# Kernel optimization log

Hardware: AMD Instinct MI355X
Metric: run time of the kernel (lower is better)

The kernel has to match this reference:

```python
import jax, jax.numpy as jnp
import numpy as np

B, T, C, H = 1024, 256, 384, 64  # batch, block_size, n_embd, head_size


def _rope_tables():
    # standard rotary tables: theta_i = 10000^(-2i/H), angles = pos * theta
    inv_freq = 1.0 / (10000.0 ** (jnp.arange(0, H, 2, dtype=jnp.float32) / H))  # [H/2]
    pos = jnp.arange(T, dtype=jnp.float32)
    ang = pos[:, None] * inv_freq[None, :]          # [T, H/2]
    ang = jnp.concatenate([ang, ang], axis=-1)       # [T, H]
    return jnp.cos(ang), jnp.sin(ang)


def setup_inputs() -> dict:
    key = jax.random.key(0)
    kx, kq, kk, kv = jax.random.split(key, 4)
    cos, sin = _rope_tables()
    s = 1.0 / np.sqrt(C)
    return {
        "x": jax.random.normal(kx, (B, T, C), dtype=jnp.float32),
        "cos": cos,
        "sin": sin,
        "Wq": jax.random.normal(kq, (C, H), dtype=jnp.float32) * s,
        "Wk": jax.random.normal(kk, (C, H), dtype=jnp.float32) * s,
        "Wv": jax.random.normal(kv, (C, H), dtype=jnp.float32) * s,
    }


def _rotary(x, cos, sin):
    # x: [B, T, H]; cos/sin: [T, H]
    half = x.shape[-1] // 2
    x1, x2 = x[..., :half], x[..., half:]
    rotated = jnp.concatenate([-x2, x1], axis=-1)
    return x * cos + rotated * sin


def reference(x, cos, sin, Wq, Wk, Wv):
    Tn = x.shape[1]
    q = x @ Wq                                  # [B,T,H]
    k = x @ Wk
    v = x @ Wv
    q = _rotary(q, cos[:Tn], sin[:Tn])
    k = _rotary(k, cos[:Tn], sin[:Tn])
    scale = k.shape[-1] ** -0.5
    wei = jnp.einsum('btd,bsd->bts', q, k) * scale  # [B,T,T] — materialized as in original
    causal = jnp.tril(jnp.ones((Tn, Tn), dtype=bool))
    wei = jnp.where(causal, wei, -jnp.inf)
    wei = jax.nn.softmax(wei, axis=-1)
    # dropout omitted (eval mode / deterministic reference)
    out = jnp.einsum('bts,bsd->btd', wei, v)    # [B,T,H]
    return out
```

## Files before the change

### kernel.cpp

```cpp
#include <hip/hip_runtime.h>
#include <hip/hip_bf16.h>


typedef __attribute__((ext_vector_type(8))) short bf16x8;
typedef __attribute__((ext_vector_type(4))) float f32x4;

#define B_ 1024
#define T_ 256
#define C_ 384
#define H_ 64

static __device__ __forceinline__ unsigned short f2bf(float f) {
  unsigned int u = __float_as_uint(f);
  return (unsigned short)((u + 0x7fffu + ((u >> 16) & 1u)) >> 16);
}

static __device__ __forceinline__ float bf2f(unsigned short h) {
  return __uint_as_float(((unsigned int)h) << 16);
}

static __device__ __forceinline__ bf16x8 cvt8(float4 a, float4 b) {
  union { __hip_bfloat162 h[4]; bf16x8 v; } u;
  u.h[0] = __float22bfloat162_rn(make_float2(a.x, a.y));
  u.h[1] = __float22bfloat162_rn(make_float2(a.z, a.w));
  u.h[2] = __float22bfloat162_rn(make_float2(b.x, b.y));
  u.h[3] = __float22bfloat162_rn(make_float2(b.z, b.w));
  return u.v;
}

__global__ void pack_w_frag(const float* __restrict__ Wq, const float* __restrict__ Wk,
                            const float* __restrict__ Wv, unsigned short* __restrict__ wtp) {
  int id = blockIdx.x * 256 + threadIdx.x;
  if (id >= 144 * 512) return;
  int i = id & 7, lane = (id >> 3) & 63, f = id >> 9;
  int nt = f % 12, ks = f / 12;
  int n = nt * 16 + (lane & 15);
  int k = ks * 32 + (lane >> 4) * 8 + i;
  const float* W = (n < 64) ? Wq : ((n < 128) ? Wk : Wv);
  wtp[id] = f2bf(W[k * 64 + (n & 63)]);
}

__launch_bounds__(256, 6)
__global__ void qkv_kernel(const float* __restrict__ x, const float* __restrict__ cosp,
                           const float* __restrict__ sinp,
                           const unsigned short* __restrict__ wtp,
                           unsigned short* __restrict__ qp,
                           unsigned short* __restrict__ kp,
                           unsigned short* __restrict__ vp) {
  __shared__ __align__(16) unsigned short xs[32 * 384];

  unsigned short* Qst = xs;
  unsigned short* Kst = xs + 2304;
  unsigned short* Vst = xs + 4608;

  const int tid = threadIdx.x;
  const int w = tid >> 6;
  const int lane = tid & 63;
  const int l15 = lane & 15;
  const int lq = lane >> 4;
  const int bk = blockIdx.x;
  const int b = bk >> 3, g32 = bk & 7;
  const int row0 = g32 * 32;

  const float* xb = x + (size_t)b * T_ * C_ + (size_t)row0 * C_;

  {
    float4 c0[2], c1[2];
    {
      const float* p = xb + (size_t)tid * 8;
      c0[0] = *(const float4*)p; c0[1] = *(const float4*)(p + 4);
    }
    #pragma unroll
    for (int s = 0; s < 6; ++s) {
      if (s + 1 < 6) {
        const float* p = xb + (size_t)((s + 1) * 256 + tid) * 8;
        c1[0] = *(const float4*)p; c1[1] = *(const float4*)(p + 4);
      }
      int c = s * 256 + tid;
      int row = c / 48;
      int cb = (c - row * 48) * 16;
      *(bf16x8*)((char*)xs + row * 768 + (cb ^ ((row & 7) << 4))) = cvt8(c0[0], c0[1]);
      c0[0] = c1[0]; c0[1] = c1[1];
    }
  }
  __syncthreads();

  const int ng = w;

  f32x4 acc[2][3];
  #pragma unroll
  for (int i = 0; i < 2; ++i)
    #pragma unroll
    for (int m = 0; m < 3; ++m) {
      f32x4 z = {0.f, 0.f, 0.f, 0.f};
      acc[i][m] = z;
    }

  const int arow0 = l15;
  const int arow1 = 16 + l15;
  const char* xrow0 = (const char*)xs + arow0 * 768;
  const char* xrow1 = (const char*)xs + arow1 * 768;
  const int asw0 = (arow0 & 7) << 4;
  const int asw1 = (arow1 & 7) << 4;

  #pragma unroll
  for (int ks = 0; ks < 12; ++ks) {
    bf16x8 bv[3];
    #pragma unroll
    for (int m = 0; m < 3; ++m)
      bv[m] = *(const bf16x8*)(wtp + ((size_t)(ks * 12 + ng * 3 + m) * 64 + lane) * 8);
    bf16x8 a0 = *(const bf16x8*)(xrow0 + ((ks * 64 + lq * 16) ^ asw0));
    bf16x8 a1 = *(const bf16x8*)(xrow1 + ((ks * 64 + lq * 16) ^ asw1));
    #pragma unroll
    for (int m = 0; m < 3; ++m) {
      acc[0][m] = __builtin_amdgcn_mfma_f32_16x16x32_bf16(a0, bv[m], acc[0][m], 0, 0, 0);
      acc[1][m] = __builtin_amdgcn_mfma_f32_16x16x32_bf16(a1, bv[m], acc[1][m], 0, 0, 0);
    }
  }
  __syncthreads();

  #pragma unroll
  for (int i = 0; i < 2; ++i) {
    #pragma unroll
    for (int m = 0; m < 3; ++m) {
      const int nt = ng * 3 + m;
      #pragma unroll
      for (int j = 0; j < 4; ++j) {
        const int r32 = i * 16 + lq * 4 + j;
        unsigned short v = f2bf(acc[i][m][j]);
        if (nt < 4)      Qst[r32 * 72 + nt * 16 + l15] = v;
        else if (nt < 8) Kst[r32 * 72 + (nt - 4) * 16 + l15] = v;
        else             Vst[((nt - 8) * 16 + l15) * 40 + r32] = v;
      }
    }
  }
  __syncthreads();

  #pragma unroll
  for (int pass = 0; pass < 3; ++pass) {
    const int id = pass * 4 + w;
    if (id < 8) {
      const unsigned short* S = (id < 4) ? Qst : Kst;
      unsigned short* dst = (id < 4) ? qp : kp;
      const int lid = id & 3;
      const int tl = lid >> 1;
      const int ks2 = lid & 1;
      const int r32 = tl * 16 + l15;
      const int c0 = ks2 * 32 + lq * 8;
      const unsigned short* rowp = S + r32 * 72;
      bf16x8 mv = *(const bf16x8*)(rowp + c0);
      bf16x8 pv = *(const bf16x8*)(rowp + (c0 ^ 32));
      const int tglob = row0 + r32;
      const float* cp = cosp + tglob * H_ + c0;
      const float* sp = sinp + tglob * H_ + c0;
      float4 ca = *(const float4*)cp, cb = *(const float4*)(cp + 4);
      float4 sa = *(const float4*)sp, sb = *(const float4*)(sp + 4);
      const float sgn = ks2 ? 1.0f : -1.0f;
      bf16x8 ov;
      ov[0] = (short)f2bf(bf2f((unsigned short)mv[0]) * ca.x + sgn * bf2f((unsigned short)pv[0]) * sa.x);
      ov[1] = (short)f2bf(bf2f((unsigned short)mv[1]) * ca.y + sgn * bf2f((unsigned short)pv[1]) * sa.y);
      ov[2] = (short)f2bf(bf2f((unsigned short)mv[2]) * ca.z + sgn * bf2f((unsigned short)pv[2]) * sa.z);
      ov[3] = (short)f2bf(bf2f((unsigned short)mv[3]) * ca.w + sgn * bf2f((unsigned short)pv[3]) * sa.w);
      ov[4] = (short)f2bf(bf2f((unsigned short)mv[4]) * cb.x + sgn * bf2f((unsigned short)pv[4]) * sb.x);
      ov[5] = (short)f2bf(bf2f((unsigned short)mv[5]) * cb.y + sgn * bf2f((unsigned short)pv[5]) * sb.y);
      ov[6] = (short)f2bf(bf2f((unsigned short)mv[6]) * cb.z + sgn * bf2f((unsigned short)pv[6]) * sb.z);
      ov[7] = (short)f2bf(bf2f((unsigned short)mv[7]) * cb.w + sgn * bf2f((unsigned short)pv[7]) * sb.w);
      const int tile_glob = g32 * 2 + tl;
      *(bf16x8*)(dst + ((((size_t)b * 16 + tile_glob) * 2 + ks2) * 64 + lane) * 8) = ov;
    } else if (id < 12) {
      const int ntv = id - 8;
      bf16x8 fr = *(const bf16x8*)(Vst + (ntv * 16 + l15) * 40 + lq * 8);
      *(bf16x8*)(vp + ((((size_t)b * 4 + ntv) * 8 + g32) * 64 + lane) * 8) = fr;
    }
  }
}

__launch_bounds__(256, 4)
__global__ void attn_kernel(const unsigned short* __restrict__ qp,
                            const unsigned short* __restrict__ kp,
                            const unsigned short* __restrict__ vp,
                            float* __restrict__ out) {
  __shared__ unsigned short Plds[4 * 16 * 264];

  const int tid = threadIdx.x;
  const int w = tid >> 6;
  const int lane = tid & 63;
  const int l15 = lane & 15;
  const int lq = lane >> 4;
  const int bk = blockIdx.x;
  const int b = bk >> 1, half = bk & 1;
  const int rt2[2] = {half * 8 + w, half * 8 + 7 - w};

  unsigned short* Pw = Plds + w * 16 * 264;
  float* ob = out + (size_t)b * T_ * H_;

  #pragma unroll
  for (int i = 0; i < 2; ++i) {
    const int ti = rt2[i];
    const int t0 = ti * 16;

    bf16x8 aq[2];
    #pragma unroll
    for (int ks2 = 0; ks2 < 2; ++ks2)
      aq[ks2] = *(const bf16x8*)(qp + ((((size_t)b * 16 + ti) * 2 + ks2) * 64 + lane) * 8);

    f32x4 sacc[16];
    #pragma unroll
    for (int si = 0; si < 16; ++si) {
      f32x4 z = {0.f, 0.f, 0.f, 0.f};
      sacc[si] = z;
    }

    #pragma unroll
    for (int si = 0; si < 16; ++si) {
      if (si <= ti) {
        #pragma unroll
        for (int ks2 = 0; ks2 < 2; ++ks2) {
          bf16x8 bkf = *(const bf16x8*)(kp + ((((size_t)b * 16 + si) * 2 + ks2) * 64 + lane) * 8);
          sacc[si] = __builtin_amdgcn_mfma_f32_16x16x32_bf16(aq[ks2], bkf, sacc[si], 0, 0, 0);
        }
      }
    }

    int trow = t0 + lq * 4;
    #pragma unroll
    for (int si = 0; si < 16; ++si) {
      #pragma unroll
      for (int j = 0; j < 4; ++j) {
        float s = sacc[si][j] * 0.125f;
        if (si * 16 + l15 > trow + j) s = -1e30f;
        sacc[si][j] = s;
      }
    }

    float rl[4];
    #pragma unroll
    for (int j = 0; j < 4; ++j) {
      float mj = -1e30f;
      #pragma unroll
      for (int si = 0; si < 16; ++si) mj = fmaxf(mj, sacc[si][j]);
      #pragma unroll
      for (int d = 1; d < 16; d <<= 1) mj = fmaxf(mj, __shfl_xor(mj, d));
      float lj = 0.0f;
      #pragma unroll
      for (int si = 0; si < 16; ++si) {
        float p = __expf(sacc[si][j] - mj);
        lj += p;
        Pw[(lq * 4 + j) * 264 + si * 16 + l15] = f2bf(p);
      }
      #pragma unroll
      for (int d = 1; d < 16; d <<= 1) lj += __shfl_xor(lj, d);
      rl[j] = 1.0f / lj;
    }

    f32x4 oacc[4];
    #pragma unroll
    for (int nt = 0; nt < 4; ++nt) {
      f32x4 z = {0.f, 0.f, 0.f, 0.f};
      oacc[nt] = z;
    }
    int nk = (t0 + 16 + 31) >> 5;
    for (int ks = 0; ks < nk; ++ks) {
      bf16x8 ap = *(const bf16x8*)&Pw[l15 * 264 + ks * 32 + lq * 8];
      #pragma unroll
      for (int nt = 0; nt < 4; ++nt) {
        bf16x8 bv = *(const bf16x8*)(vp + ((((size_t)b * 4 + nt) * 8 + ks) * 64 + lane) * 8);
        oacc[nt] = __builtin_amdgcn_mfma_f32_16x16x32_bf16(ap, bv, oacc[nt], 0, 0, 0);
      }
    }

    #pragma unroll
    for (int nt = 0; nt < 4; ++nt)
      #pragma unroll
      for (int j = 0; j < 4; ++j)
        ob[(t0 + lq * 4 + j) * H_ + nt * 16 + l15] = oacc[nt][j] * rl[j];
  }
}

extern "C" void kernel_launch(void* const* d_in, const int* in_sizes, int n_in,
                              void* d_out, int out_size, void* d_ws, size_t ws_size,
                              hipStream_t stream) {
  const float* x    = (const float*)d_in[0];
  const float* cosp = (const float*)d_in[1];
  const float* sinp = (const float*)d_in[2];
  const float* Wq   = (const float*)d_in[3];
  const float* Wk   = (const float*)d_in[4];
  const float* Wv   = (const float*)d_in[5];
  float* out = (float*)d_out;

  const size_t wtp_bytes = 144 * 512 * 2;
  const size_t frag_elems = (size_t)B_ * 16 * 2 * 64 * 8;

  unsigned short* wtp = (unsigned short*)d_ws;
  unsigned short* qp = (unsigned short*)((char*)d_ws + wtp_bytes);
  unsigned short* kp = qp + frag_elems;
  unsigned short* vp = kp + frag_elems;
  (void)ws_size;

  pack_w_frag<<<288, 256, 0, stream>>>(Wq, Wk, Wv, wtp);
  qkv_kernel<<<B_ * 8, 256, 0, stream>>>(x, cosp, sinp, wtp, qp, kp, vp);
  attn_kernel<<<B_ * 2, 256, 0, stream>>>(qp, kp, vp, out);
}
```

Before: 222.4 us.

## Stage fp32 x tile via direct global-to-LDS loads, convert to bf16 on read

Replaces the register-staged fp32-to-bf16 conversion of the x tile with async global_load_lds copies that write raw fp32 into LDS, using a swizzled source address so LDS reads stay conflict-free. The bf16 conversion moves into the MFMA loop, where each A fragment is built from two float4 LDS reads. This doubles LDS usage to 48KB per block, so launch bounds drop from 6 to 3 blocks per SM, trading occupancy for fewer VGPR round trips during the load. It also adds conversion work to the inner loop.

```diff
diff --git a/kernel.cpp b/kernel.cpp
--- a/kernel.cpp
+++ b/kernel.cpp
@@ -17,6 +17,11 @@
 
 static __device__ __forceinline__ float bf2f(unsigned short h) {
   return __uint_as_float(((unsigned int)h) << 16);
+}
+
+static __device__ __forceinline__ void glds16(const void* g, void* l) {
+  __builtin_amdgcn_global_load_lds((const __attribute__((address_space(1))) void*)g,
+                                   (__attribute__((address_space(3))) void*)l, 16, 0, 0);
 }
 
 static __device__ __forceinline__ bf16x8 cvt8(float4 a, float4 b) {
@@ -40,18 +45,18 @@
   wtp[id] = f2bf(W[k * 64 + (n & 63)]);
 }
 
-__launch_bounds__(256, 6)
+__launch_bounds__(256, 3)
 __global__ void qkv_kernel(const float* __restrict__ x, const float* __restrict__ cosp,
                            const float* __restrict__ sinp,
                            const unsigned short* __restrict__ wtp,
                            unsigned short* __restrict__ qp,
                            unsigned short* __restrict__ kp,
                            unsigned short* __restrict__ vp) {
-  __shared__ __align__(16) unsigned short xs[32 * 384];
-
-  unsigned short* Qst = xs;
-  unsigned short* Kst = xs + 2304;
-  unsigned short* Vst = xs + 4608;
+  __shared__ __align__(16) float xs[32 * 384];
+
+  unsigned short* Qst = (unsigned short*)xs;
+  unsigned short* Kst = (unsigned short*)xs + 2304;
+  unsigned short* Vst = (unsigned short*)xs + 4608;
 
   const int tid = threadIdx.x;
   const int w = tid >> 6;
@@ -62,27 +67,18 @@
   const int b = bk >> 3, g32 = bk & 7;
   const int row0 = g32 * 32;
 
-  const float* xb = x + (size_t)b * T_ * C_ + (size_t)row0 * C_;
-
-  {
-    float4 c0[2], c1[2];
-    {
-      const float* p = xb + (size_t)tid * 8;
-      c0[0] = *(const float4*)p; c0[1] = *(const float4*)(p + 4);
-    }
-    #pragma unroll
-    for (int s = 0; s < 6; ++s) {
-      if (s + 1 < 6) {
-        const float* p = xb + (size_t)((s + 1) * 256 + tid) * 8;
-        c1[0] = *(const float4*)p; c1[1] = *(const float4*)(p + 4);
-      }
-      int c = s * 256 + tid;
-      int row = c / 48;
-      int cb = (c - row * 48) * 16;
-      *(bf16x8*)((char*)xs + row * 768 + (cb ^ ((row & 7) << 4))) = cvt8(c0[0], c0[1]);
-      c0[0] = c1[0]; c0[1] = c1[1];
-    }
-  }
+  const char* xbc = (const char*)(x + (size_t)b * T_ * C_ + (size_t)row0 * C_);
+
+  #pragma unroll
+  for (int s = 0; s < 12; ++s) {
+    const int cbase = s * 256 + w * 64;
+    const int c = cbase + lane;
+    const int row = c / 96;
+    const int cb = (c - row * 96) * 16;
+    const char* src = xbc + row * 1536 + (cb ^ ((row & 7) << 4));
+    glds16(src, (char*)xs + cbase * 16);
+  }
+  asm volatile("s_waitcnt vmcnt(0)" ::: "memory");
   __syncthreads();
 
   const int ng = w;
@@ -96,25 +92,29 @@
       acc[i][m] = z;
     }
 
-  const int arow0 = l15;
-  const int arow1 = 16 + l15;
-  const char* xrow0 = (const char*)xs + arow0 * 768;
-  const char* xrow1 = (const char*)xs + arow1 * 768;
-  const int asw0 = (arow0 & 7) << 4;
-  const int asw1 = (arow1 & 7) << 4;
-
   #pragma unroll
   for (int ks = 0; ks < 12; ++ks) {
     bf16x8 bv[3];
     #pragma unroll
     for (int m = 0; m < 3; ++m)
       bv[m] = *(const bf16x8*)(wtp + ((size_t)(ks * 12 + ng * 3 + m) * 64 + lane) * 8);
-    bf16x8 a0 = *(const bf16x8*)(xrow0 + ((ks * 64 + lq * 16) ^ asw0));
-    bf16x8 a1 = *(const bf16x8*)(xrow1 + ((ks * 64 + lq * 16) ^ asw1));
+
+    bf16x8 af[2];
+    #pragma unroll
+    for (int i = 0; i < 2; ++i) {
+      const int R = i * 16 + l15;
+      const int swz = (R & 7) << 4;
+      const char* base = (const char*)xs + R * 1536;
+      const int cbyte = ks * 128 + lq * 32;
+      float4 f0 = *(const float4*)(base + (cbyte ^ swz));
+      float4 f1 = *(const float4*)(base + ((cbyte + 16) ^ swz));
+      af[i] = cvt8(f0, f1);
+    }
+
     #pragma unroll
     for (int m = 0; m < 3; ++m) {
-      acc[0][m] = __builtin_amdgcn_mfma_f32_16x16x32_bf16(a0, bv[m], acc[0][m], 0, 0, 0);
-      acc[1][m] = __builtin_amdgcn_mfma_f32_16x16x32_bf16(a1, bv[m], acc[1][m], 0, 0, 0);
+      acc[0][m] = __builtin_amdgcn_mfma_f32_16x16x32_bf16(af[0], bv[m], acc[0][m], 0, 0, 0);
+      acc[1][m] = __builtin_amdgcn_mfma_f32_16x16x32_bf16(af[1], bv[m], acc[1][m], 0, 0, 0);
     }
   }
   __syncthreads();
```

Result: slower. 248.1 us (+11.5%).
